# Kernel tuning notes

Hardware: AMD Instinct MI355X
Metric: run time of the kernel (lower is better)

Reference implementation:

```python
import jax, jax.numpy as jnp
import numpy as np

WINDOW = 3
RATIO = 5


def _box_filter(x, win):
    """Depthwise 3D box (mean) filter, 'same' padding, per channel.
    x: [N, C, D, H, W] -> [N, C, D, H, W]
    Matches torch conv3d with ones([1,1,w,w,w])/w^3 applied per channel.
    """
    c = x.shape[1]
    k = jnp.ones((c, 1, win, win, win), x.dtype) / (win ** 3)
    pad = win // 2
    return jax.lax.conv_general_dilated(
        x, k,
        window_strides=(1, 1, 1),
        padding=[(pad, pad)] * 3,
        dimension_numbers=('NCDHW', 'OIDHW', 'NCDHW'),
        feature_group_count=c,
    )


def setup_inputs() -> dict:
    key = jax.random.key(0)
    k1, k2 = jax.random.split(key)
    y_pred = jax.random.normal(k1, (1, 3, 192, 192, 192), dtype=jnp.float32)
    y_true = jax.random.uniform(k2, (1, 1, 192, 192, 192), dtype=jnp.float32)
    return {"y_pred": y_pred, "y_true": y_true}


def reference(y_pred, y_true):
    # Finite differences (abs), each [1, 3, D-1, H-1, W-1]
    base = y_pred[:, :, :-1, :-1, :-1]
    dy = jnp.abs(y_pred[:, :, 1:, :-1, :-1] - base)
    dx = jnp.abs(y_pred[:, :, :-1, 1:, :-1] - base)
    dz = jnp.abs(y_pred[:, :, :-1, :-1, 1:] - base)

    # 9 box-filtered single-channel maps == 3 depthwise box filters
    fx = _box_filter(dx, WINDOW)
    fy = _box_filter(dy, WINDOW)
    fz = _box_filter(dz, WINDOW)
    dxdx, dxdy, dxdz = fx[:, 1:2], fy[:, 1:2], fz[:, 1:2]
    dydx, dydy, dydz = fx[:, 0:1], fy[:, 0:1], fz[:, 0:1]
    dzdx, dzdy, dzdz = fx[:, 2:3], fy[:, 2:3], fz[:, 2:3]

    # Neo-Hookean invariants
    det_1 = (dxdx + 1) * ((dydy + 1) * (dzdz + 1) - dydz * dzdy)
    det_2 = -dxdy * (dydx * (dzdz + 1) - dydz * dzdx)
    det_3 = dxdz * (dydx * dzdy - (dydy + 1) * dzdx)
    J = det_1 + det_2 + det_3

    Tr = ((dxdx + 1) ** 2 + dxdy ** 2 + dxdz ** 2
          + dydx ** 2 + (dydy + 1) ** 2 + dydz ** 2
          + dzdx ** 2 + dzdy ** 2 + (dzdz + 1) ** 2)

    # mode == 'exp'
    stretch = Tr * jnp.exp(-J + 1) - 3
    vol_change = (J - 1) ** 2

    # Faithful replication of the sequential mu/lambda normalization in torch:
    mu = 1.0
    lam = mu * RATIO
    mu = mu / (mu + lam)          # 1/6
    lam = lam / (mu + lam)        # 30/31 (uses updated mu, as in source)

    U = mu / 2 * stretch + lam / 2 * vol_change
    return jnp.mean(U)
```

## Files before the change

kernel.cpp:

```cpp
#include <hip/hip_runtime.h>
#include <math.h>

#define DIM 192
#define OD  191
#define PLANE 36864
#define VOL 7077888
#define TW  14
#define TH  16
#define CD  16
#define NBW 14
#define NBH 12
#define NCH 12

typedef float    f4 __attribute__((ext_vector_type(4)));
typedef _Float16 h8 __attribute__((ext_vector_type(8)));
typedef _Float16 h2 __attribute__((ext_vector_type(2)));

template<int CTRL>
__device__ __forceinline__ int dppi(int x) {
    return __builtin_amdgcn_update_dpp(0, x, CTRL, 0xF, 0xF, true);
}

union U8 { h8 v; int i[4]; };
union U2 { h2 v; int i; };

__device__ __forceinline__ void wsum3(h8& a, h2& b) {
    U8 ua, s1, s2;
    ua.v = a;
    #pragma unroll
    for (int k = 0; k < 4; ++k) {
        s1.i[k] = dppi<0x101>(ua.i[k]);
        s2.i[k] = dppi<0x111>(ua.i[k]);
    }
    a = ua.v + s1.v + s2.v;
    U2 ub, t1, t2;
    ub.v = b;
    t1.i = dppi<0x101>(ub.i);
    t2.i = dppi<0x111>(ub.i);
    b = ub.v + t1.v + t2.v;
}

__device__ __forceinline__ void make_diff(const f4 c, const f4 cw, const f4 ch, const f4 cd,
                                          h8& va, h2& vb) {
    const float hx  = fabsf(ch.x - c.x), hy  = fabsf(ch.y - c.y), hz  = fabsf(ch.z - c.z);
    const float dx_ = fabsf(cd.x - c.x), dy_ = fabsf(cd.y - c.y), dz_ = fabsf(cd.z - c.z);
    const float wx  = fabsf(cw.x - c.x), wy  = fabsf(cw.y - c.y), wz  = fabsf(cw.z - c.z);
    va = (h8){(_Float16)hx,  (_Float16)hy,  (_Float16)hz,
              (_Float16)dx_, (_Float16)dy_, (_Float16)dz_,
              (_Float16)wx,  (_Float16)wy};
    vb = (h2){(_Float16)wz, (_Float16)0.f};
}

__device__ __forceinline__ f4 ld3(const float* __restrict__ P, int idx, bool ok) {
    f4 r = (f4)0;
    if (ok) {
        r.x = P[idx];
        r.y = P[idx + VOL];
        r.z = P[idx + 2 * VOL];
    }
    return r;
}

__global__ __launch_bounds__(256, 7)
void nh_fused_kernel(const float* __restrict__ P, float* __restrict__ out) {
    const int tid = threadIdx.x;
    const int tx  = tid & 15;
    const int ty  = tid >> 4;
    const int w0  = blockIdx.x * TW;
    const int h0  = blockIdx.y * TH;
    const int ds  = blockIdx.z * CD;
    const int de  = min(ds + CD, OD);

    __shared__ f4 sraw[2][19][18];
    __shared__ h8 sW[2][18][16];
    __shared__ h2 sWB[2][18][16];
    __shared__ float wsum[4];

    const int hp_p = h0 - 1 + ty;
    const int wp_p = w0 - 1 + tx;
    const bool in_raw_p  = (hp_p >= 0) & (hp_p < DIM) & (wp_p >= 0) & (wp_p < DIM);
    const bool in_diff_p = (hp_p >= 0) & (hp_p < OD)  & (wp_p >= 0) & (wp_p < OD);
    const int base_p = hp_p * DIM + wp_p;

    int hh_l, ww_l;
    if (tid < 48) { hh_l = 16 + (tid >> 4); ww_l = tid & 15; }
    else          { hh_l = tid - 48;        ww_l = 16; }
    const bool has_l = (tid < 67);
    const int hp_l = h0 - 1 + hh_l;
    const int wp_l = w0 - 1 + ww_l;
    const bool in_raw_l  = has_l & (hp_l >= 0) & (hp_l < DIM) & (wp_l >= 0) & (wp_l < DIM);
    const bool in_diff_l = (tid < 32) & (hp_l >= 0) & (hp_l < OD) & (wp_l >= 0) & (wp_l < OD);
    const int base_l = hp_l * DIM + wp_l;

    const bool valid = (tx < TW) && (w0 + tx < OD) && (h0 + ty < OD);

    h8 a0 = (h8)0, a1 = (h8)0, a2 = (h8)0;
    h2 b0 = (h2)0, b1 = (h2)0, b2 = (h2)0;
    f4 cur_p = (f4)0, prev_p = (f4)0;
    f4 cur_l = (f4)0, prev_l = (f4)0;
    float acc = 0.f;

    {
        const int t0 = ds - 1;
        if (t0 >= 0) {
            cur_p = ld3(P, t0 * PLANE + base_p, in_raw_p);
            cur_l = ld3(P, t0 * PLANE + base_l, in_raw_l);
        }
    }

    for (int t = ds - 1; t <= de + 1; ++t) {
        const int cb = t & 1, pb = cb ^ 1;

        f4 nxt_p = (f4)0, nxt_l = (f4)0;
        {
            const int tn = t + 1;
            if ((tn < DIM) & (tn <= de + 1)) {
                nxt_p = ld3(P, tn * PLANE + base_p, in_raw_p);
                nxt_l = ld3(P, tn * PLANE + base_l, in_raw_l);
            }
        }

        sraw[cb][ty][tx] = cur_p;
        if (has_l) sraw[cb][hh_l][ww_l] = cur_l;

        const bool built = (t >= ds) & (t - 1 >= 0) & (t - 1 < OD);

        {
            h8 sa = (h8)0; h2 sb = (h2)0;
            if (built) {
                h8 va = (h8)0; h2 vb = (h2)0;
                if (in_diff_p) {
                    const f4 c  = prev_p;
                    const f4 cw = sraw[pb][ty][tx + 1];
                    const f4 ch = sraw[pb][ty + 1][tx];
                    const f4 cd = cur_p;
                    make_diff(c, cw, ch, cd, va, vb);
                }
                wsum3(va, vb);
                sa = va; sb = vb;
            }
            sW[cb][ty][tx] = sa; sWB[cb][ty][tx] = sb;
        }
        if (tid < 32) {
            h8 sa = (h8)0; h2 sb = (h2)0;
            if (built) {
                h8 va = (h8)0; h2 vb = (h2)0;
                if (in_diff_l) {
                    const f4 c  = prev_l;
                    const f4 cw = sraw[pb][hh_l][ww_l + 1];
                    const f4 ch = sraw[pb][hh_l + 1][ww_l];
                    const f4 cd = cur_l;
                    make_diff(c, cw, ch, cd, va, vb);
                }
                wsum3(va, vb);
                sa = va; sb = vb;
            }
            sW[cb][hh_l][ww_l] = sa; sWB[cb][hh_l][ww_l] = sb;
        }

        __syncthreads();

        a0 = a1; a1 = a2; b0 = b1; b1 = b2;
        {
            const int cc = (tx + 1) & 15;
            a2 = sW[cb][ty][cc] + sW[cb][ty + 1][cc] + sW[cb][ty + 2][cc];
            b2 = sWB[cb][ty][cc] + sWB[cb][ty + 1][cc] + sWB[cb][ty + 2][cc];
        }

        const int d = t - 2;
        if (valid && d >= ds && d < de) {
            const h8 FA = a0 + a1 + a2;
            const h2 FB = b0 + b1 + b2;
            const float inv27 = 1.f / 27.f;
            const float dydx = (float)FA[0] * inv27, dxdx = (float)FA[1] * inv27, dzdx = (float)FA[2] * inv27;
            const float dydy = (float)FA[3] * inv27, dxdy = (float)FA[4] * inv27, dzdy = (float)FA[5] * inv27;
            const float dydz = (float)FA[6] * inv27, dxdz = (float)FA[7] * inv27, dzdz = (float)FB[0] * inv27;
            const float a = dxdx + 1.f, e = dydy + 1.f, iN = dzdz + 1.f;
            const float J = a * (e * iN - dydz * dzdy)
                          - dxdy * (dydx * iN - dydz * dzdx)
                          + dxdz * (dydx * dzdy - e * dzdx);
            const float Tr = a * a + dxdy * dxdy + dxdz * dxdz
                           + dydx * dydx + e * e + dydz * dydz
                           + dzdx * dzdx + dzdy * dzdy + iN * iN;
            const float stretch = Tr * expf(1.f - J) - 3.f;
            const float vol = (J - 1.f) * (J - 1.f);
            acc += 0.0833333358f * stretch + 0.4838709677f * vol;
        }

        prev_p = cur_p; cur_p = nxt_p;
        prev_l = cur_l; cur_l = nxt_l;
    }

    acc *= (1.f / 6967871.f);

    #pragma unroll
    for (int off = 32; off > 0; off >>= 1) acc += __shfl_down(acc, off, 64);
    if ((tid & 63) == 0) wsum[tid >> 6] = acc;
    __syncthreads();
    if (tid == 0) {
        atomicAdd(out, wsum[0] + wsum[1] + wsum[2] + wsum[3]);
    }
}

extern "C" void kernel_launch(void* const* d_in, const int* in_sizes, int n_in,
                              void* d_out, int out_size, void* d_ws, size_t ws_size,
                              hipStream_t stream) {
    const float* y_pred = (const float*)d_in[0];
    float* out = (float*)d_out;

    hipMemsetAsync(out, 0, sizeof(float), stream);

    dim3 grid(NBW, NBH, NCH);
    nh_fused_kernel<<<grid, 256, 0, stream>>>(y_pred, out);
}
```

Before: 173.6 us.

## Stage raw planes in fp16, spread halo work across waves, use fast exp

```diff
diff --git a/kernel.cpp b/kernel.cpp
--- a/kernel.cpp
+++ b/kernel.cpp
@@ -14,6 +14,7 @@
 
 typedef float    f4 __attribute__((ext_vector_type(4)));
 typedef _Float16 h8 __attribute__((ext_vector_type(8)));
+typedef _Float16 h4 __attribute__((ext_vector_type(4)));
 typedef _Float16 h2 __attribute__((ext_vector_type(2)));
 
 template<int CTRL>
@@ -40,28 +41,25 @@
     b = ub.v + t1.v + t2.v;
 }
 
-__device__ __forceinline__ void make_diff(const f4 c, const f4 cw, const f4 ch, const f4 cd,
-                                          h8& va, h2& vb) {
-    const float hx  = fabsf(ch.x - c.x), hy  = fabsf(ch.y - c.y), hz  = fabsf(ch.z - c.z);
-    const float dx_ = fabsf(cd.x - c.x), dy_ = fabsf(cd.y - c.y), dz_ = fabsf(cd.z - c.z);
-    const float wx  = fabsf(cw.x - c.x), wy  = fabsf(cw.y - c.y), wz  = fabsf(cw.z - c.z);
-    va = (h8){(_Float16)hx,  (_Float16)hy,  (_Float16)hz,
-              (_Float16)dx_, (_Float16)dy_, (_Float16)dz_,
-              (_Float16)wx,  (_Float16)wy};
-    vb = (h2){(_Float16)wz, (_Float16)0.f};
-}
-
-__device__ __forceinline__ f4 ld3(const float* __restrict__ P, int idx, bool ok) {
-    f4 r = (f4)0;
+__device__ __forceinline__ void make_diff16(const h4 c, const h4 cw, const h4 ch, const h4 cd,
+                                            h8& va, h2& vb) {
+    const h4 dh = __builtin_elementwise_abs(ch - c);
+    const h4 dd = __builtin_elementwise_abs(cd - c);
+    const h4 dw = __builtin_elementwise_abs(cw - c);
+    va = (h8){dh[0], dh[1], dh[2], dd[0], dd[1], dd[2], dw[0], dw[1]};
+    vb = (h2){dw[2], (_Float16)0.f};
+}
+
+__device__ __forceinline__ h4 ld3h(const float* __restrict__ P, int idx, bool ok) {
+    h4 r = (h4)0;
     if (ok) {
-        r.x = P[idx];
-        r.y = P[idx + VOL];
-        r.z = P[idx + 2 * VOL];
+        r = (h4){(_Float16)P[idx], (_Float16)P[idx + VOL], (_Float16)P[idx + 2 * VOL],
+                 (_Float16)0.f};
     }
     return r;
 }
 
-__global__ __launch_bounds__(256, 7)
+__global__ __launch_bounds__(256, 8)
 void nh_fused_kernel(const float* __restrict__ P, float* __restrict__ out) {
     const int tid = threadIdx.x;
     const int tx  = tid & 15;
@@ -71,7 +69,7 @@
     const int ds  = blockIdx.z * CD;
     const int de  = min(ds + CD, OD);
 
-    __shared__ f4 sraw[2][19][18];
+    __shared__ h4 sraw[2][19][18];
     __shared__ h8 sW[2][18][16];
     __shared__ h2 sWB[2][18][16];
     __shared__ float wsum[4];
@@ -82,41 +80,44 @@
     const bool in_diff_p = (hp_p >= 0) & (hp_p < OD)  & (wp_p >= 0) & (wp_p < OD);
     const int base_p = hp_p * DIM + wp_p;
 
-    int hh_l, ww_l;
-    if (tid < 48) { hh_l = 16 + (tid >> 4); ww_l = tid & 15; }
-    else          { hh_l = tid - 48;        ww_l = 16; }
-    const bool has_l = (tid < 67);
+    int hh_l = 0, ww_l = 0;
+    bool has_l = false, build2 = false;
+    if      (tid >= 64  && tid < 80)  { hh_l = 16;        ww_l = tid - 64;  has_l = true; build2 = true; }
+    else if (tid >= 128 && tid < 144) { hh_l = 17;        ww_l = tid - 128; has_l = true; build2 = true; }
+    else if (tid >= 192 && tid < 208) { hh_l = 18;        ww_l = tid - 192; has_l = true; }
+    else if (tid >= 208 && tid < 227) { hh_l = tid - 208; ww_l = 16;       has_l = true; }
     const int hp_l = h0 - 1 + hh_l;
     const int wp_l = w0 - 1 + ww_l;
-    const bool in_raw_l  = has_l & (hp_l >= 0) & (hp_l < DIM) & (wp_l >= 0) & (wp_l < DIM);
-    const bool in_diff_l = (tid < 32) & (hp_l >= 0) & (hp_l < OD) & (wp_l >= 0) & (wp_l < OD);
+    const bool in_raw_l  = has_l  & (hp_l >= 0) & (hp_l < DIM) & (wp_l >= 0) & (wp_l < DIM);
+    const bool in_diff_l = build2 & (hp_l >= 0) & (hp_l < OD)  & (wp_l >= 0) & (wp_l < OD);
     const int base_l = hp_l * DIM + wp_l;
 
     const bool valid = (tx < TW) && (w0 + tx < OD) && (h0 + ty < OD);
 
     h8 a0 = (h8)0, a1 = (h8)0, a2 = (h8)0;
     h2 b0 = (h2)0, b1 = (h2)0, b2 = (h2)0;
-    f4 cur_p = (f4)0, prev_p = (f4)0;
-    f4 cur_l = (f4)0, prev_l = (f4)0;
+    h4 cur_p = (h4)0, prev_p = (h4)0;
+    h4 cur_l = (h4)0, prev_l = (h4)0;
     float acc = 0.f;
 
     {
         const int t0 = ds - 1;
         if (t0 >= 0) {
-            cur_p = ld3(P, t0 * PLANE + base_p, in_raw_p);
-            cur_l = ld3(P, t0 * PLANE + base_l, in_raw_l);
-        }
-    }
-
+            cur_p = ld3h(P, t0 * PLANE + base_p, in_raw_p);
+            if (has_l) cur_l = ld3h(P, t0 * PLANE + base_l, in_raw_l);
+        }
+    }
+
+    #pragma unroll 3
     for (int t = ds - 1; t <= de + 1; ++t) {
         const int cb = t & 1, pb = cb ^ 1;
 
-        f4 nxt_p = (f4)0, nxt_l = (f4)0;
+        h4 nxt_p = (h4)0, nxt_l = (h4)0;
         {
             const int tn = t + 1;
             if ((tn < DIM) & (tn <= de + 1)) {
-                nxt_p = ld3(P, tn * PLANE + base_p, in_raw_p);
-                nxt_l = ld3(P, tn * PLANE + base_l, in_raw_l);
+                nxt_p = ld3h(P, tn * PLANE + base_p, in_raw_p);
+                if (has_l) nxt_l = ld3h(P, tn * PLANE + base_l, in_raw_l);
             }
         }
 
@@ -130,27 +131,25 @@
             if (built) {
                 h8 va = (h8)0; h2 vb = (h2)0;
                 if (in_diff_p) {
-                    const f4 c  = prev_p;
-                    const f4 cw = sraw[pb][ty][tx + 1];
-                    const f4 ch = sraw[pb][ty + 1][tx];
-                    const f4 cd = cur_p;
-                    make_diff(c, cw, ch, cd, va, vb);
+                    make_diff16(prev_p,
+                                sraw[pb][ty][tx + 1],
+                                sraw[pb][ty + 1][tx],
+                                cur_p, va, vb);
                 }
                 wsum3(va, vb);
                 sa = va; sb = vb;
             }
             sW[cb][ty][tx] = sa; sWB[cb][ty][tx] = sb;
         }
-        if (tid < 32) {
+        if (build2) {
             h8 sa = (h8)0; h2 sb = (h2)0;
             if (built) {
                 h8 va = (h8)0; h2 vb = (h2)0;
                 if (in_diff_l) {
-                    const f4 c  = prev_l;
-                    const f4 cw = sraw[pb][hh_l][ww_l + 1];
-                    const f4 ch = sraw[pb][hh_l + 1][ww_l];
-                    const f4 cd = cur_l;
-                    make_diff(c, cw, ch, cd, va, vb);
+                    make_diff16(prev_l,
+                                sraw[pb][hh_l][ww_l + 1],
+                                sraw[pb][hh_l + 1][ww_l],
+                                cur_l, va, vb);
                 }
                 wsum3(va, vb);
                 sa = va; sb = vb;
@@ -182,7 +181,7 @@
             const float Tr = a * a + dxdy * dxdy + dxdz * dxdz
                            + dydx * dydx + e * e + dydz * dydz
                            + dzdx * dzdx + dzdy * dzdy + iN * iN;
-            const float stretch = Tr * expf(1.f - J) - 3.f;
+            const float stretch = Tr * __expf(1.f - J) - 3.f;
             const float vol = (J - 1.f) * (J - 1.f);
             acc += 0.0833333358f * stretch + 0.4838709677f * vol;
         }
```

New measurement: 183.1 us. 1.05x slower.
